# Kernel tuning notes

Hardware: AMD Instinct MI355X
Metric: run time of the kernel (lower is better)

Reference implementation:

```python
import jax, jax.numpy as jnp
import numpy as np

EPS = 1e-7
ALPHA = 16.0
RANK = 64
CURV = 1.0


def lorentz_expmap0(x, c):
    # x: [N, d] tangent at origin (spatial part). Returns [N, d+1] point on hyperboloid.
    sc = jnp.sqrt(c)
    vn = jnp.maximum(jnp.linalg.norm(x, axis=-1, keepdims=True), EPS)  # [N,1]
    t = jnp.cosh(sc * vn) / sc                                        # [N,1] time coord
    sp = (jnp.sinh(sc * vn) / (sc * vn)) * x                          # [N,d] spatial
    return jnp.concatenate([t, sp], axis=-1)


def lorentz_recompute_time(s, c):
    # s: [N, d] spatial part. time = sqrt(1/c + ||s||^2) so <p,p>_L = -1/c.
    sq = jnp.sum(s * s, axis=-1, keepdims=True)
    t = jnp.sqrt(1.0 / c + sq)
    return jnp.concatenate([t, s], axis=-1)


def lorentz_logmap0(p, c):
    # p: [N, d+1] on hyperboloid. Returns [N, d] tangent (spatial) at origin.
    sc = jnp.sqrt(c)
    t = p[:, :1]
    y = p[:, 1:]
    yn = jnp.maximum(jnp.linalg.norm(y, axis=-1, keepdims=True), EPS)
    arg = jnp.maximum(sc * t, 1.0 + EPS)  # arccosh domain clamp
    d = jnp.arccosh(arg) / sc             # geodesic distance from origin
    return (d / yn) * y


def setup_inputs() -> dict:
    key = jax.random.key(0)
    k1, k2, k3 = jax.random.split(key, 3)
    N, D_IN, D_OUT, R = 16384, 4096, 4096, RANK
    x = jax.random.normal(k1, (N, D_IN), dtype=jnp.float32) * 0.02
    # torch Linear weight layout: A_w [r, in], B_w [out, r]
    A_w = jax.random.normal(k2, (R, D_IN), dtype=jnp.float32) * (1.0 / np.sqrt(D_IN))
    B_w = jax.random.normal(k3, (D_OUT, R), dtype=jnp.float32) * (1.0 / np.sqrt(R))
    return {"x": x, "A_w": A_w, "B_w": B_w}


def reference(x, A_w, B_w):
    c = CURV
    p0 = lorentz_expmap0(x, c)                    # [N, D_IN+1]
    s1 = p0[:, 1:] @ A_w.T                        # [N, R]
    p1 = lorentz_recompute_time(s1, c)            # [N, R+1]
    s2 = p1[:, 1:] @ B_w.T                        # [N, D_OUT]
    p2 = lorentz_recompute_time(s2, c)            # [N, D_OUT+1]
    v = lorentz_logmap0(p2, c)                    # [N, D_OUT]
    return (ALPHA / RANK) * v
```

## Files before the change

### kernel.cpp

```cpp
#include <hip/hip_runtime.h>
#include <hip/hip_bf16.h>

#define NROWS 16384
#define DIN   4096
#define DOUT  4096
#define RNK   64
#define EPSF  1e-7f

typedef float  f32x4  __attribute__((ext_vector_type(4)));
typedef __bf16 bf16x4 __attribute__((ext_vector_type(4)));
typedef __bf16 bf16x8 __attribute__((ext_vector_type(8)));

__device__ __forceinline__ bf16x8 cvt8(f32x4 a, f32x4 b) {
    bf16x8 r;
    r[0]=(__bf16)a.x; r[1]=(__bf16)a.y; r[2]=(__bf16)a.z; r[3]=(__bf16)a.w;
    r[4]=(__bf16)b.x; r[5]=(__bf16)b.y; r[6]=(__bf16)b.z; r[7]=(__bf16)b.w;
    return r;
}

#define LPK 136
__global__ __launch_bounds__(512, 4)
void k1_expmap_gemm1(const float* __restrict__ x, const float* __restrict__ Aw,
                     float* __restrict__ s1) {
    __shared__ __bf16 xs[32][LPK];
    __shared__ __bf16 as[64][LPK];
    __shared__ float rowss[32];

    const int t = threadIdx.x;
    const int l = t & 63;
    const int w = t >> 6;
    const int brow = blockIdx.x * 32;

    const int xrow = t >> 4, xcol = (t & 15) * 8;
    const int arow = t >> 3, acol = (t & 7) * 16;
    const size_t xb = (size_t)(brow + xrow) * DIN + xcol;
    const size_t ab = (size_t)arow * DIN + acol;

    const int m0 = (w & 1) * 16;
    const int n0 = (w >> 1) * 16;
    const int frow = l & 15;
    const int koff = (l >> 4) * 8;

    float ssq = 0.f;
    f32x4 acc = {0.f, 0.f, 0.f, 0.f};

    f32x4 xA0,xA1,aA0,aA1,aA2,aA3, xB0,xB1,aB0,aB1,aB2,aB3;

    auto load = [&](f32x4&x0,f32x4&x1,f32x4&A0,f32x4&A1,f32x4&A2,f32x4&A3,int kt){
        const size_t o = (size_t)kt * 128;
        x0 = *(const f32x4*)&x[xb + o];       x1 = *(const f32x4*)&x[xb + o + 4];
        A0 = *(const f32x4*)&Aw[ab + o];      A1 = *(const f32x4*)&Aw[ab + o + 4];
        A2 = *(const f32x4*)&Aw[ab + o + 8];  A3 = *(const f32x4*)&Aw[ab + o + 12];
    };
    auto consume = [&](const f32x4&x0,const f32x4&x1,const f32x4&A0,
                       const f32x4&A1,const f32x4&A2,const f32x4&A3){
        ssq += x0.x*x0.x + x0.y*x0.y + x0.z*x0.z + x0.w*x0.w;
        ssq += x1.x*x1.x + x1.y*x1.y + x1.z*x1.z + x1.w*x1.w;
        *(bf16x8*)&xs[xrow][xcol]     = cvt8(x0, x1);
        *(bf16x8*)&as[arow][acol]     = cvt8(A0, A1);
        *(bf16x8*)&as[arow][acol + 8] = cvt8(A2, A3);
        __syncthreads();
        #pragma unroll
        for (int ks = 0; ks < 4; ++ks) {
            bf16x8 af = *(const bf16x8*)&xs[m0 + frow][ks*32 + koff];
            bf16x8 bf_ = *(const bf16x8*)&as[n0 + frow][ks*32 + koff];
            acc = __builtin_amdgcn_mfma_f32_16x16x32_bf16(af, bf_, acc, 0, 0, 0);
        }
        __syncthreads();
    };

    const int NT = DIN / 128;
    load(xA0,xA1,aA0,aA1,aA2,aA3, 0);
    for (int kt = 0; kt < NT; kt += 2) {
        load(xB0,xB1,aB0,aB1,aB2,aB3, kt + 1);
        consume(xA0,xA1,aA0,aA1,aA2,aA3);
        if (kt + 2 < NT) load(xA0,xA1,aA0,aA1,aA2,aA3, kt + 2);
        consume(xB0,xB1,aB0,aB1,aB2,aB3);
    }

    ssq += __shfl_xor(ssq, 1);
    ssq += __shfl_xor(ssq, 2);
    ssq += __shfl_xor(ssq, 4);
    ssq += __shfl_xor(ssq, 8);
    if ((l & 15) == 0) rowss[w * 4 + (l >> 4)] = ssq;
    __syncthreads();
    if (t < 32) {
        float vn = fmaxf(sqrtf(rowss[t]), EPSF);
        rowss[t] = sinhf(vn) / vn;
    }
    __syncthreads();

    #pragma unroll
    for (int q = 0; q < 4; ++q) {
        const int row = m0 + (l >> 4) * 4 + q;
        s1[(size_t)(brow + row) * RNK + n0 + frow] = rowss[row] * acc[q];
    }
}

__global__ __launch_bounds__(512, 4)
void kb_gram(const float* __restrict__ Bw, __bf16* __restrict__ Bp,
             float* __restrict__ Gpart) {
    __shared__ __bf16 bs[256][72];
    const int t = threadIdx.x;
    const int jb = blockIdx.x * 256;

    {
        const int j0 = t >> 1, c0 = (t & 1) * 32;
        #pragma unroll
        for (int u = 0; u < 4; ++u) {
            f32x4 v0 = *(const f32x4*)&Bw[(size_t)(jb + j0) * RNK + c0 + 8*u];
            f32x4 v1 = *(const f32x4*)&Bw[(size_t)(jb + j0) * RNK + c0 + 8*u + 4];
            bf16x8 p = cvt8(v0, v1);
            *(bf16x8*)&bs[j0][c0 + 8*u] = p;
            *(bf16x8*)&Bp[(size_t)(jb + j0) * RNK + c0 + 8*u] = p;
        }
    }
    __syncthreads();

    const int r = t & 63, rp = (t >> 6) * 8;
    float acc[8] = {0,0,0,0,0,0,0,0};
    for (int j = 0; j < 256; ++j) {
        float s = (float)bs[j][r];
        bf16x8 v = *(const bf16x8*)&bs[j][rp];
        #pragma unroll
        for (int u = 0; u < 8; ++u) acc[u] += s * (float)v[u];
    }
    #pragma unroll
    for (int u = 0; u < 8; ++u)
        Gpart[(size_t)blockIdx.x * 4096 + r * 64 + rp + u] = acc[u];
}

__global__ void kc0_sum(const float* __restrict__ Gpart, float* __restrict__ G) {
    const int t = threadIdx.x;
    #pragma unroll
    for (int v = 0; v < 4; ++v) {
        f32x4 a = {0.f, 0.f, 0.f, 0.f};
        for (int b = 0; b < 16; ++b)
            a += *(const f32x4*)&Gpart[(size_t)b * 4096 + t * 16 + v * 4];
        *(f32x4*)&G[t * 16 + v * 4] = a;
    }
}

__global__ __launch_bounds__(512, 4)
void kc_scale(const float* __restrict__ s1, const float* __restrict__ G,
              __bf16* __restrict__ s1p) {
    __shared__ float Gs[64][64];
    __shared__ float sr[8][64];
    const int t = threadIdx.x, l = t & 63, w = t >> 6;

    {
        float* gf = &Gs[0][0];
        *(f32x4*)&gf[t * 8]     = *(const f32x4*)&G[t * 8];
        *(f32x4*)&gf[t * 8 + 4] = *(const f32x4*)&G[t * 8 + 4];
    }
    const int row = blockIdx.x * 8 + w;
    const float a = s1[(size_t)row * RNK + l];
    sr[w][l] = a;
    __syncthreads();

    float y = 0.f;
    #pragma unroll 8
    for (int r = 0; r < 64; ++r) y += Gs[r][l] * sr[w][r];

    float q = a * y;
    q += __shfl_xor(q, 1);  q += __shfl_xor(q, 2);  q += __shfl_xor(q, 4);
    q += __shfl_xor(q, 8);  q += __shfl_xor(q, 16); q += __shfl_xor(q, 32);

    const float r2 = q;
    const float rn = sqrtf(r2);
    const float g = 0.25f * acoshf(fmaxf(sqrtf(1.f + r2), 1.f + EPSF))
                          / fmaxf(rn, EPSF);
    s1p[(size_t)row * RNK + l] = (__bf16)(g * a);
}

__global__ __launch_bounds__(512, 4)
void k2_gemm2(const __bf16* __restrict__ s1p, const __bf16* __restrict__ Bp,
              float* __restrict__ out) {
    __shared__ __bf16 ss[64][72];
    __shared__ __bf16 bsh[64][72];
    const int t = threadIdx.x, l = t & 63, w = t >> 6;
    const int rt = blockIdx.x >> 6;
    const int ct = blockIdx.x & 63;
    const int brow = rt * 64, bcol = ct * 64;

    {
        const int row = t >> 3, c = (t & 7) * 8;
        *(bf16x8*)&ss[row][c]  = *(const bf16x8*)&s1p[(size_t)(brow + row) * RNK + c];
        *(bf16x8*)&bsh[row][c] = *(const bf16x8*)&Bp[(size_t)(bcol + row) * RNK + c];
    }
    __syncthreads();

    const int m0 = (w & 3) * 16;
    const int n0 = (w >> 2) * 32;
    const int frow = l & 15;
    const int koff = (l >> 4) * 8;

    f32x4 a0 = {0.f,0.f,0.f,0.f}, a1 = {0.f,0.f,0.f,0.f};
    #pragma unroll
    for (int ks = 0; ks < 2; ++ks) {
        bf16x8 af = *(const bf16x8*)&ss[m0 + frow][ks*32 + koff];
        bf16x8 b0 = *(const bf16x8*)&bsh[n0 + frow][ks*32 + koff];
        bf16x8 b1 = *(const bf16x8*)&bsh[n0 + 16 + frow][ks*32 + koff];
        a0 = __builtin_amdgcn_mfma_f32_16x16x32_bf16(af, b0, a0, 0, 0, 0);
        a1 = __builtin_amdgcn_mfma_f32_16x16x32_bf16(af, b1, a1, 0, 0, 0);
    }

    #pragma unroll
    for (int q = 0; q < 4; ++q) {
        const int row = m0 + (l >> 4) * 4 + q;
        const size_t ob = (size_t)(brow + row) * DOUT + bcol;
        out[ob + n0 + frow]      = a0[q];
        out[ob + n0 + 16 + frow] = a1[q];
    }
}

extern "C" void kernel_launch(void* const* d_in, const int* in_sizes, int n_in,
                              void* d_out, int out_size, void* d_ws, size_t ws_size,
                              hipStream_t stream) {
    const float* x  = (const float*)d_in[0];
    const float* Aw = (const float*)d_in[1];
    const float* Bw = (const float*)d_in[2];
    float* out = (float*)d_out;

    char* ws = (char*)d_ws;
    float*  s1    = (float*)(ws);
    __bf16* s1p   = (__bf16*)(ws + 4194304);
    __bf16* Bp    = (__bf16*)(ws + 6291456);
    float*  Gpart = (float*)(ws + 6815744);
    float*  G     = (float*)(ws + 7077888);

    k1_expmap_gemm1<<<NROWS / 32, 512, 0, stream>>>(x, Aw, s1);
    kb_gram<<<16, 512, 0, stream>>>(Bw, Bp, Gpart);
    kc0_sum<<<1, 256, 0, stream>>>(Gpart, G);
    kc_scale<<<NROWS / 8, 512, 0, stream>>>(s1, G, s1p);
    k2_gemm2<<<16384, 512, 0, stream>>>(s1p, Bp, out);
}
```

Baseline: 169.5 us.

## Fuse expmap GEMM1, Gram-based scaling and GEMM2 into one kernel

Merges the first GEMM, the per-row Gram-matrix norm scaling and the second GEMM into a single kernel per 32-row block. The s1/s1p intermediates stay in shared memory instead of round-tripping through global memory, which also removes two kernel launches. B is pre-packed into MFMA fragment order so the fused kernel can load B fragments straight from global without staging them in LDS. The trade-off is a much larger LDS footprint per block, which may lower occupancy, and the output-write phase now runs inside the long-running GEMM1 blocks with scattered column stores.

```diff
diff --git a/kernel.cpp b/kernel.cpp
--- a/kernel.cpp
+++ b/kernel.cpp
@@ -18,32 +18,95 @@
     return r;
 }
 
+__global__ __launch_bounds__(512, 4)
+void kb_gram(const float* __restrict__ Bw, __bf16* __restrict__ Bpf,
+             float* __restrict__ Gpart) {
+    __shared__ __bf16 bs[256][72];
+    const int t = threadIdx.x;
+    const int jb = blockIdx.x * 256;
+
+    {
+        const int j0 = t >> 1, c0 = (t & 1) * 32;
+        #pragma unroll
+        for (int u = 0; u < 4; ++u) {
+            f32x4 v0 = *(const f32x4*)&Bw[(size_t)(jb + j0) * RNK + c0 + 8*u];
+            f32x4 v1 = *(const f32x4*)&Bw[(size_t)(jb + j0) * RNK + c0 + 8*u + 4];
+            *(bf16x8*)&bs[j0][c0 + 8*u] = cvt8(v0, v1);
+        }
+    }
+    __syncthreads();
+
+    #pragma unroll
+    for (int u = 0; u < 4; ++u) {
+        const int lc = t + 512 * u;
+        const int ll = lc & 63;
+        const int ks = (lc >> 6) & 1;
+        const int jl = lc >> 7;
+        bf16x8 v = *(const bf16x8*)&bs[jl * 16 + (ll & 15)][ks * 32 + (ll >> 4) * 8];
+        const size_t C = ((size_t)((jb >> 4) + jl) * 2 + ks) * 64 + ll;
+        *(bf16x8*)&Bpf[C * 8] = v;
+    }
+
+    const int r = t & 63, rp = (t >> 6) * 8;
+    float acc[8] = {0,0,0,0,0,0,0,0};
+    for (int j = 0; j < 256; ++j) {
+        float s = (float)bs[j][r];
+        bf16x8 v = *(const bf16x8*)&bs[j][rp];
+        #pragma unroll
+        for (int u = 0; u < 8; ++u) acc[u] += s * (float)v[u];
+    }
+    #pragma unroll
+    for (int u = 0; u < 8; ++u)
+        Gpart[(size_t)blockIdx.x * 4096 + r * 64 + rp + u] = acc[u];
+}
+
+__global__ void kc0_sum(const float* __restrict__ Gpart, float* __restrict__ G) {
+    const int t = threadIdx.x;
+    #pragma unroll
+    for (int v = 0; v < 4; ++v) {
+        f32x4 a = {0.f, 0.f, 0.f, 0.f};
+        for (int b = 0; b < 16; ++b)
+            a += *(const f32x4*)&Gpart[(size_t)b * 4096 + t * 16 + v * 4];
+        *(f32x4*)&G[t * 16 + v * 4] = a;
+    }
+}
+
 #define LPK 136
 __global__ __launch_bounds__(512, 4)
-void k1_expmap_gemm1(const float* __restrict__ x, const float* __restrict__ Aw,
-                     float* __restrict__ s1) {
+void kfused(const float* __restrict__ x, const float* __restrict__ Aw,
+            const float* __restrict__ G, const __bf16* __restrict__ Bpf,
+            float* __restrict__ out) {
     __shared__ __bf16 xs[32][LPK];
     __shared__ __bf16 as[64][LPK];
-    __shared__ float rowss[32];
+    __shared__ float  Gs[64][64];
+    __shared__ float  s1f[32][64];
+    __shared__ __bf16 s1pf[2][2][64][8];
+    __shared__ float  rowss[32];
+    __shared__ float  gs[32];
 
     const int t = threadIdx.x;
     const int l = t & 63;
     const int w = t >> 6;
     const int brow = blockIdx.x * 32;
 
+    {
+        float* gf = &Gs[0][0];
+        *(f32x4*)&gf[t * 8]     = *(const f32x4*)&G[t * 8];
+        *(f32x4*)&gf[t * 8 + 4] = *(const f32x4*)&G[t * 8 + 4];
+    }
+
     const int xrow = t >> 4, xcol = (t & 15) * 8;
     const int arow = t >> 3, acol = (t & 7) * 16;
     const size_t xb = (size_t)(brow + xrow) * DIN + xcol;
     const size_t ab = (size_t)arow * DIN + acol;
 
-    const int m0 = (w & 1) * 16;
-    const int n0 = (w >> 1) * 16;
+    const int m0   = (w & 1) * 16;
+    const int n0   = (w >> 1) * 16;
     const int frow = l & 15;
     const int koff = (l >> 4) * 8;
 
     float ssq = 0.f;
     f32x4 acc = {0.f, 0.f, 0.f, 0.f};
-
     f32x4 xA0,xA1,aA0,aA1,aA2,aA3, xB0,xB1,aB0,aB1,aB2,aB3;
 
     auto load = [&](f32x4&x0,f32x4&x1,f32x4&A0,f32x4&A1,f32x4&A2,f32x4&A3,int kt){
@@ -62,7 +125,7 @@
         __syncthreads();
         #pragma unroll
         for (int ks = 0; ks < 4; ++ks) {
-            bf16x8 af = *(const bf16x8*)&xs[m0 + frow][ks*32 + koff];
+            bf16x8 af  = *(const bf16x8*)&xs[m0 + frow][ks*32 + koff];
             bf16x8 bf_ = *(const bf16x8*)&as[n0 + frow][ks*32 + koff];
             acc = __builtin_amdgcn_mfma_f32_16x16x32_bf16(af, bf_, acc, 0, 0, 0);
         }
@@ -93,124 +156,77 @@
     #pragma unroll
     for (int q = 0; q < 4; ++q) {
         const int row = m0 + (l >> 4) * 4 + q;
-        s1[(size_t)(brow + row) * RNK + n0 + frow] = rowss[row] * acc[q];
-    }
-}
-
-__global__ __launch_bounds__(512, 4)
-void kb_gram(const float* __restrict__ Bw, __bf16* __restrict__ Bp,
-             float* __restrict__ Gpart) {
-    __shared__ __bf16 bs[256][72];
-    const int t = threadIdx.x;
-    const int jb = blockIdx.x * 256;
-
-    {
-        const int j0 = t >> 1, c0 = (t & 1) * 32;
-        #pragma unroll
-        for (int u = 0; u < 4; ++u) {
-            f32x4 v0 = *(const f32x4*)&Bw[(size_t)(jb + j0) * RNK + c0 + 8*u];
-            f32x4 v1 = *(const f32x4*)&Bw[(size_t)(jb + j0) * RNK + c0 + 8*u + 4];
-            bf16x8 p = cvt8(v0, v1);
-            *(bf16x8*)&bs[j0][c0 + 8*u] = p;
-            *(bf16x8*)&Bp[(size_t)(jb + j0) * RNK + c0 + 8*u] = p;
-        }
-    }
-    __syncthreads();
-
-    const int r = t & 63, rp = (t >> 6) * 8;
-    float acc[8] = {0,0,0,0,0,0,0,0};
-    for (int j = 0; j < 256; ++j) {
-        float s = (float)bs[j][r];
-        bf16x8 v = *(const bf16x8*)&bs[j][rp];
-        #pragma unroll
-        for (int u = 0; u < 8; ++u) acc[u] += s * (float)v[u];
-    }
-    #pragma unroll
-    for (int u = 0; u < 8; ++u)
-        Gpart[(size_t)blockIdx.x * 4096 + r * 64 + rp + u] = acc[u];
-}
-
-__global__ void kc0_sum(const float* __restrict__ Gpart, float* __restrict__ G) {
-    const int t = threadIdx.x;
-    #pragma unroll
-    for (int v = 0; v < 4; ++v) {
-        f32x4 a = {0.f, 0.f, 0.f, 0.f};
-        for (int b = 0; b < 16; ++b)
-            a += *(const f32x4*)&Gpart[(size_t)b * 4096 + t * 16 + v * 4];
-        *(f32x4*)&G[t * 16 + v * 4] = a;
-    }
-}
-
-__global__ __launch_bounds__(512, 4)
-void kc_scale(const float* __restrict__ s1, const float* __restrict__ G,
-              __bf16* __restrict__ s1p) {
-    __shared__ float Gs[64][64];
-    __shared__ float sr[8][64];
-    const int t = threadIdx.x, l = t & 63, w = t >> 6;
-
-    {
-        float* gf = &Gs[0][0];
-        *(f32x4*)&gf[t * 8]     = *(const f32x4*)&G[t * 8];
-        *(f32x4*)&gf[t * 8 + 4] = *(const f32x4*)&G[t * 8 + 4];
-    }
-    const int row = blockIdx.x * 8 + w;
-    const float a = s1[(size_t)row * RNK + l];
-    sr[w][l] = a;
-    __syncthreads();
-
-    float y = 0.f;
-    #pragma unroll 8
-    for (int r = 0; r < 64; ++r) y += Gs[r][l] * sr[w][r];
-
-    float q = a * y;
-    q += __shfl_xor(q, 1);  q += __shfl_xor(q, 2);  q += __shfl_xor(q, 4);
-    q += __shfl_xor(q, 8);  q += __shfl_xor(q, 16); q += __shfl_xor(q, 32);
-
-    const float r2 = q;
-    const float rn = sqrtf(r2);
-    const float g = 0.25f * acoshf(fmaxf(sqrtf(1.f + r2), 1.f + EPSF))
-                          / fmaxf(rn, EPSF);
-    s1p[(size_t)row * RNK + l] = (__bf16)(g * a);
-}
-
-__global__ __launch_bounds__(512, 4)
-void k2_gemm2(const __bf16* __restrict__ s1p, const __bf16* __restrict__ Bp,
-              float* __restrict__ out) {
-    __shared__ __bf16 ss[64][72];
-    __shared__ __bf16 bsh[64][72];
-    const int t = threadIdx.x, l = t & 63, w = t >> 6;
-    const int rt = blockIdx.x >> 6;
-    const int ct = blockIdx.x & 63;
-    const int brow = rt * 64, bcol = ct * 64;
-
-    {
-        const int row = t >> 3, c = (t & 7) * 8;
-        *(bf16x8*)&ss[row][c]  = *(const bf16x8*)&s1p[(size_t)(brow + row) * RNK + c];
-        *(bf16x8*)&bsh[row][c] = *(const bf16x8*)&Bp[(size_t)(bcol + row) * RNK + c];
-    }
-    __syncthreads();
-
-    const int m0 = (w & 3) * 16;
-    const int n0 = (w >> 2) * 32;
-    const int frow = l & 15;
-    const int koff = (l >> 4) * 8;
-
-    f32x4 a0 = {0.f,0.f,0.f,0.f}, a1 = {0.f,0.f,0.f,0.f};
-    #pragma unroll
-    for (int ks = 0; ks < 2; ++ks) {
-        bf16x8 af = *(const bf16x8*)&ss[m0 + frow][ks*32 + koff];
-        bf16x8 b0 = *(const bf16x8*)&bsh[n0 + frow][ks*32 + koff];
-        bf16x8 b1 = *(const bf16x8*)&bsh[n0 + 16 + frow][ks*32 + koff];
-        a0 = __builtin_amdgcn_mfma_f32_16x16x32_bf16(af, b0, a0, 0, 0, 0);
-        a1 = __builtin_amdgcn_mfma_f32_16x16x32_bf16(af, b1, a1, 0, 0, 0);
-    }
-
-    #pragma unroll
-    for (int q = 0; q < 4; ++q) {
-        const int row = m0 + (l >> 4) * 4 + q;
-        const size_t ob = (size_t)(brow + row) * DOUT + bcol;
-        out[ob + n0 + frow]      = a0[q];
-        out[ob + n0 + 16 + frow] = a1[q];
+        s1f[row][n0 + frow] = rowss[row] * acc[q];
+    }
+    __syncthreads();
+
+    {
+        const int r0 = w * 4;
+        float y0=0.f, y1=0.f, y2=0.f, y3=0.f;
+        for (int r = 0; r < 64; ++r) {
+            const float gr = Gs[r][l];
+            y0 += gr * s1f[r0 + 0][r];
+            y1 += gr * s1f[r0 + 1][r];
+            y2 += gr * s1f[r0 + 2][r];
+            y3 += gr * s1f[r0 + 3][r];
+        }
+        float q0 = s1f[r0 + 0][l] * y0;
+        float q1 = s1f[r0 + 1][l] * y1;
+        float q2 = s1f[r0 + 2][l] * y2;
+        float q3 = s1f[r0 + 3][l] * y3;
+        #pragma unroll
+        for (int s = 1; s < 64; s <<= 1) {
+            q0 += __shfl_xor(q0, s);
+            q1 += __shfl_xor(q1, s);
+            q2 += __shfl_xor(q2, s);
+            q3 += __shfl_xor(q3, s);
+        }
+        if (l == 0) {
+            float r2v[4] = {q0, q1, q2, q3};
+            #pragma unroll
+            for (int i = 0; i < 4; ++i) {
+                const float r2 = r2v[i];
+                const float rn = sqrtf(r2);
+                gs[r0 + i] = 0.25f * acoshf(fmaxf(sqrtf(1.f + r2), 1.f + EPSF))
+                                   / fmaxf(rn, EPSF);
+            }
+        }
+    }
+    __syncthreads();
+
+    if (t < 256) {
+        const int ll = t & 63, ksq = (t >> 6) & 1, mg = t >> 7;
+        const int row = mg * 16 + (ll & 15);
+        const int kc  = ksq * 32 + (ll >> 4) * 8;
+        const float gg = gs[row];
+        bf16x8 p;
+        #pragma unroll
+        for (int u = 0; u < 8; ++u) p[u] = (__bf16)(gg * s1f[row][kc + u]);
+        *(bf16x8*)&s1pf[mg][ksq][ll][0] = p;
+    }
+    __syncthreads();
+
+    {
+        const int mg = w & 1;
+        const int mr0 = mg * 16;
+        const bf16x8 a0f = *(const bf16x8*)&s1pf[mg][0][l][0];
+        const bf16x8 a1f = *(const bf16x8*)&s1pf[mg][1][l][0];
+        #pragma unroll 4
+        for (int jj = 0; jj < 64; ++jj) {
+            const int j = (w >> 1) + jj * 4;
+            const size_t base = ((size_t)j * 2 * 64 + l) * 8;
+            bf16x8 b0 = *(const bf16x8*)&Bpf[base];
+            bf16x8 b1 = *(const bf16x8*)&Bpf[base + 512];
+            f32x4 a2 = {0.f, 0.f, 0.f, 0.f};
+            a2 = __builtin_amdgcn_mfma_f32_16x16x32_bf16(a0f, b0, a2, 0, 0, 0);
+            a2 = __builtin_amdgcn_mfma_f32_16x16x32_bf16(a1f, b1, a2, 0, 0, 0);
+            const int col = j * 16 + frow;
+            #pragma unroll
+            for (int q = 0; q < 4; ++q) {
+                const int row = mr0 + (l >> 4) * 4 + q;
+                out[(size_t)(brow + row) * DOUT + col] = a2[q];
+            }
+        }
     }
 }
 
@@ -223,15 +239,11 @@
     float* out = (float*)d_out;
 
     char* ws = (char*)d_ws;
-    float*  s1    = (float*)(ws);
-    __bf16* s1p   = (__bf16*)(ws + 4194304);
-    __bf16* Bp    = (__bf16*)(ws + 6291456);
-    float*  Gpart = (float*)(ws + 6815744);
-    float*  G     = (float*)(ws + 7077888);
-
-    k1_expmap_gemm1<<<NROWS / 32, 512, 0, stream>>>(x, Aw, s1);
-    kb_gram<<<16, 512, 0, stream>>>(Bw, Bp, Gpart);
+    __bf16* Bpf   = (__bf16*)(ws);
+    float*  Gpart = (float*)(ws + 524288);
+    float*  G     = (float*)(ws + 786432);
+
+    kb_gram<<<16, 512, 0, stream>>>(Bw, Bpf, Gpart);
     kc0_sum<<<1, 256, 0, stream>>>(Gpart, G);
-    kc_scale<<<NROWS / 8, 512, 0, stream>>>(s1, G, s1p);
-    k2_gemm2<<<16384, 512, 0, stream>>>(s1p, Bp, out);
-}
+    kfused<<<NROWS / 32, 512, 0, stream>>>(x, Aw, G, Bpf, out);
+}
```

New measurement: 182.5 us. +7.7%, slower.

## Restructure GEMM1 with split-K waves and pre-packed bf16 A fragments

Applied to the files above, without the earlier changes.

Adds a small kernel that converts A_w to bf16 once per call, already laid out in MFMA fragment order. The first GEMM now uses 16-row blocks with a four-way split-K across waves: each wave streams its own K slice of x with register double-buffering and reads A fragments directly from global memory, so A no longer goes through shared memory. Partial results are reduced in shared memory and written as bf16, which halves the intermediate traffic. The cost is an extra launch, a cross-wave reduction step, and lower precision in the intermediate s1.

```diff
diff --git a/kernel.cpp b/kernel.cpp
--- a/kernel.cpp
+++ b/kernel.cpp
@@ -17,84 +17,19 @@
     r[4]=(__bf16)b.x; r[5]=(__bf16)b.y; r[6]=(__bf16)b.z; r[7]=(__bf16)b.w;
     return r;
 }
-
-#define LPK 136
-__global__ __launch_bounds__(512, 4)
-void k1_expmap_gemm1(const float* __restrict__ x, const float* __restrict__ Aw,
-                     float* __restrict__ s1) {
-    __shared__ __bf16 xs[32][LPK];
-    __shared__ __bf16 as[64][LPK];
-    __shared__ float rowss[32];
-
+__device__ __forceinline__ bf16x4 cvt4(f32x4 v) {
+    bf16x4 r;
+    r[0]=(__bf16)v.x; r[1]=(__bf16)v.y; r[2]=(__bf16)v.z; r[3]=(__bf16)v.w;
+    return r;
+}
+
+__global__ __launch_bounds__(512, 2)
+void ka_apf(const float* __restrict__ Aw, __bf16* __restrict__ Apf) {
+    const int kt = blockIdx.x;
     const int t = threadIdx.x;
-    const int l = t & 63;
-    const int w = t >> 6;
-    const int brow = blockIdx.x * 32;
-
-    const int xrow = t >> 4, xcol = (t & 15) * 8;
-    const int arow = t >> 3, acol = (t & 7) * 16;
-    const size_t xb = (size_t)(brow + xrow) * DIN + xcol;
-    const size_t ab = (size_t)arow * DIN + acol;
-
-    const int m0 = (w & 1) * 16;
-    const int n0 = (w >> 1) * 16;
-    const int frow = l & 15;
-    const int koff = (l >> 4) * 8;
-
-    float ssq = 0.f;
-    f32x4 acc = {0.f, 0.f, 0.f, 0.f};
-
-    f32x4 xA0,xA1,aA0,aA1,aA2,aA3, xB0,xB1,aB0,aB1,aB2,aB3;
-
-    auto load = [&](f32x4&x0,f32x4&x1,f32x4&A0,f32x4&A1,f32x4&A2,f32x4&A3,int kt){
-        const size_t o = (size_t)kt * 128;
-        x0 = *(const f32x4*)&x[xb + o];       x1 = *(const f32x4*)&x[xb + o + 4];
-        A0 = *(const f32x4*)&Aw[ab + o];      A1 = *(const f32x4*)&Aw[ab + o + 4];
-        A2 = *(const f32x4*)&Aw[ab + o + 8];  A3 = *(const f32x4*)&Aw[ab + o + 12];
-    };
-    auto consume = [&](const f32x4&x0,const f32x4&x1,const f32x4&A0,
-                       const f32x4&A1,const f32x4&A2,const f32x4&A3){
-        ssq += x0.x*x0.x + x0.y*x0.y + x0.z*x0.z + x0.w*x0.w;
-        ssq += x1.x*x1.x + x1.y*x1.y + x1.z*x1.z + x1.w*x1.w;
-        *(bf16x8*)&xs[xrow][xcol]     = cvt8(x0, x1);
-        *(bf16x8*)&as[arow][acol]     = cvt8(A0, A1);
-        *(bf16x8*)&as[arow][acol + 8] = cvt8(A2, A3);
-        __syncthreads();
-        #pragma unroll
-        for (int ks = 0; ks < 4; ++ks) {
-            bf16x8 af = *(const bf16x8*)&xs[m0 + frow][ks*32 + koff];
-            bf16x8 bf_ = *(const bf16x8*)&as[n0 + frow][ks*32 + koff];
-            acc = __builtin_amdgcn_mfma_f32_16x16x32_bf16(af, bf_, acc, 0, 0, 0);
-        }
-        __syncthreads();
-    };
-
-    const int NT = DIN / 128;
-    load(xA0,xA1,aA0,aA1,aA2,aA3, 0);
-    for (int kt = 0; kt < NT; kt += 2) {
-        load(xB0,xB1,aB0,aB1,aB2,aB3, kt + 1);
-        consume(xA0,xA1,aA0,aA1,aA2,aA3);
-        if (kt + 2 < NT) load(xA0,xA1,aA0,aA1,aA2,aA3, kt + 2);
-        consume(xB0,xB1,aB0,aB1,aB2,aB3);
-    }
-
-    ssq += __shfl_xor(ssq, 1);
-    ssq += __shfl_xor(ssq, 2);
-    ssq += __shfl_xor(ssq, 4);
-    ssq += __shfl_xor(ssq, 8);
-    if ((l & 15) == 0) rowss[w * 4 + (l >> 4)] = ssq;
-    __syncthreads();
-    if (t < 32) {
-        float vn = fmaxf(sqrtf(rowss[t]), EPSF);
-        rowss[t] = sinhf(vn) / vn;
-    }
-    __syncthreads();
-
-    #pragma unroll
-    for (int q = 0; q < 4; ++q) {
-        const int row = m0 + (l >> 4) * 4 + q;
-        s1[(size_t)(brow + row) * RNK + n0 + frow] = rowss[row] * acc[q];
-    }
+    const int ng = t >> 7, le = (t >> 1) & 63, h = t & 1;
+    f32x4 v = *(const f32x4*)&Aw[(size_t)(ng*16 + (le&15)) * DIN + kt*32 + (le>>4)*8 + h*4];
+    *(bf16x4*)&Apf[((size_t)(kt*4 + ng))*512 + le*8 + h*4] = cvt4(v);
 }
 
 __global__ __launch_bounds__(512, 4)
@@ -103,7 +38,6 @@
     __shared__ __bf16 bs[256][72];
     const int t = threadIdx.x;
     const int jb = blockIdx.x * 256;
-
     {
         const int j0 = t >> 1, c0 = (t & 1) * 32;
         #pragma unroll
@@ -116,7 +50,6 @@
         }
     }
     __syncthreads();
-
     const int r = t & 63, rp = (t >> 6) * 8;
     float acc[8] = {0,0,0,0,0,0,0,0};
     for (int j = 0; j < 256; ++j) {
@@ -141,20 +74,110 @@
     }
 }
 
+__global__ __launch_bounds__(256, 3)
+void k1(const float* __restrict__ x, const __bf16* __restrict__ Apf,
+        __bf16* __restrict__ s1b) {
+    __shared__ __align__(16) char smem[37120];
+    float (*part)[16][68] = (float (*)[16][68])(smem);
+    float (*ssqs)[16]     = (float (*)[16])(smem + 36864);
+
+    const int tid = threadIdx.x, l = tid & 63, w = tid >> 6;
+    const int brow = blockIdx.x * 16;
+    const int rlo = l >> 5;
+    const int c32 = (l & 31) * 4;
+
+    __bf16* stg = (__bf16*)(smem + w * 9216);
+    const size_t xbase = (size_t)brow * DIN + (size_t)w * 1024;
+
+    f32x4 cur[8], nxt[8];
+    f32x4 acc[4];
+    #pragma unroll
+    for (int n = 0; n < 4; ++n) acc[n] = (f32x4){0.f, 0.f, 0.f, 0.f};
+    float ssqp[8] = {0.f,0.f,0.f,0.f,0.f,0.f,0.f,0.f};
+
+    #pragma unroll
+    for (int j = 0; j < 8; ++j)
+        cur[j] = *(const f32x4*)&x[xbase + (size_t)(2*j + rlo) * DIN + c32];
+
+    #pragma unroll
+    for (int t = 0; t < 8; ++t) {
+        bf16x8 ap[16];
+        #pragma unroll
+        for (int kk = 0; kk < 4; ++kk) {
+            #pragma unroll
+            for (int ng = 0; ng < 4; ++ng) {
+                const int kt = w * 32 + t * 4 + kk;
+                ap[kk*4 + ng] = *(const bf16x8*)&Apf[((size_t)(kt*4 + ng))*512 + l*8];
+            }
+        }
+        if (t < 7) {
+            #pragma unroll
+            for (int j = 0; j < 8; ++j)
+                nxt[j] = *(const f32x4*)&x[xbase + (size_t)(2*j + rlo) * DIN
+                                           + (size_t)(t+1)*128 + c32];
+        }
+        __bf16* buf = stg + (t & 1) * 2304;
+        #pragma unroll
+        for (int j = 0; j < 8; ++j) {
+            f32x4 v = cur[j];
+            ssqp[j] += v.x*v.x + v.y*v.y + v.z*v.z + v.w*v.w;
+            *(bf16x4*)&buf[(2*j + rlo) * 144 + c32] = cvt4(v);
+        }
+        #pragma unroll
+        for (int kk = 0; kk < 4; ++kk) {
+            bf16x8 af = *(const bf16x8*)&buf[(l & 15)*144 + kk*32 + (l >> 4)*8];
+            #pragma unroll
+            for (int ng = 0; ng < 4; ++ng)
+                acc[ng] = __builtin_amdgcn_mfma_f32_16x16x32_bf16(ap[kk*4+ng], af,
+                                                                  acc[ng], 0, 0, 0);
+        }
+        if (t < 7) {
+            #pragma unroll
+            for (int j = 0; j < 8; ++j) cur[j] = nxt[j];
+        }
+    }
+
+    #pragma unroll
+    for (int j = 0; j < 8; ++j) {
+        float v = ssqp[j];
+        v += __shfl_xor(v, 1);  v += __shfl_xor(v, 2);  v += __shfl_xor(v, 4);
+        v += __shfl_xor(v, 8);  v += __shfl_xor(v, 16);
+        if ((l & 31) == 0) ssqs[w][2*j + rlo] = v;
+    }
+    __syncthreads();
+
+    const int rl = l & 15, ko = l >> 4;
+    *(f32x4*)&part[w][rl][ 0 + ko*4] = acc[0];
+    *(f32x4*)&part[w][rl][16 + ko*4] = acc[1];
+    *(f32x4*)&part[w][rl][32 + ko*4] = acc[2];
+    *(f32x4*)&part[w][rl][48 + ko*4] = acc[3];
+    __syncthreads();
+
+    const int row = tid >> 4, c4 = (tid & 15) * 4;
+    f32x4 s = *(const f32x4*)&part[0][row][c4];
+    s += *(const f32x4*)&part[1][row][c4];
+    s += *(const f32x4*)&part[2][row][c4];
+    s += *(const f32x4*)&part[3][row][c4];
+    const float ssqt = ssqs[0][row] + ssqs[1][row] + ssqs[2][row] + ssqs[3][row];
+    const float vn = fmaxf(sqrtf(ssqt), EPSF);
+    const float sc = sinhf(vn) / vn;
+    s *= sc;
+    *(bf16x4*)&s1b[(size_t)(brow + row) * RNK + c4] = cvt4(s);
+}
+
 __global__ __launch_bounds__(512, 4)
-void kc_scale(const float* __restrict__ s1, const float* __restrict__ G,
+void kc_scale(const __bf16* __restrict__ s1b, const float* __restrict__ G,
               __bf16* __restrict__ s1p) {
     __shared__ float Gs[64][64];
     __shared__ float sr[8][64];
     const int t = threadIdx.x, l = t & 63, w = t >> 6;
-
     {
         float* gf = &Gs[0][0];
         *(f32x4*)&gf[t * 8]     = *(const f32x4*)&G[t * 8];
         *(f32x4*)&gf[t * 8 + 4] = *(const f32x4*)&G[t * 8 + 4];
     }
     const int row = blockIdx.x * 8 + w;
-    const float a = s1[(size_t)row * RNK + l];
+    const float a = (float)s1b[(size_t)row * RNK + l];
     sr[w][l] = a;
     __syncthreads();
 
@@ -223,15 +246,17 @@
     float* out = (float*)d_out;
 
     char* ws = (char*)d_ws;
-    float*  s1    = (float*)(ws);
-    __bf16* s1p   = (__bf16*)(ws + 4194304);
-    __bf16* Bp    = (__bf16*)(ws + 6291456);
-    float*  Gpart = (float*)(ws + 6815744);
-    float*  G     = (float*)(ws + 7077888);
-
-    k1_expmap_gemm1<<<NROWS / 32, 512, 0, stream>>>(x, Aw, s1);
+    __bf16* Apf   = (__bf16*)(ws);
+    __bf16* Bp    = (__bf16*)(ws + 0x080000);
+    float*  Gpart = (float*)(ws + 0x100000);
+    float*  G     = (float*)(ws + 0x140000);
+    __bf16* s1b   = (__bf16*)(ws + 0x150000);
+    __bf16* s1p   = (__bf16*)(ws + 0x350000);
+
+    ka_apf<<<128, 512, 0, stream>>>(Aw, Apf);
     kb_gram<<<16, 512, 0, stream>>>(Bw, Bp, Gpart);
     kc0_sum<<<1, 256, 0, stream>>>(Gpart, G);
-    kc_scale<<<NROWS / 8, 512, 0, stream>>>(s1, G, s1p);
+    k1<<<NROWS / 16, 256, 0, stream>>>(x, Apf, s1b);
+    kc_scale<<<NROWS / 8, 512, 0, stream>>>(s1b, G, s1p);
     k2_gemm2<<<16384, 512, 0, stream>>>(s1p, Bp, out);
 }
```

Measured after the change: 309.9 us. 1.83x slower.
